# Kernel tuning notes

Hardware: AMD Instinct MI355X
Metric: run time of the kernel (lower is better)

## Reference

```python
import jax, jax.numpy as jnp
import numpy as np

E = 32          # n_routed_experts / num_local_experts
H = 1024        # hidden_size
I = 512         # moe_intermediate_size
G = 8           # n_group
TKG = 4         # topk_group
TOPK = 8        # num_experts_per_tok
NSH = 2         # n_shared_experts
SCALE = 2.5     # routed_scaling_factor


def setup_inputs() -> dict:
    key = jax.random.key(0)
    ks = jax.random.split(key, 10)
    s = 0.02
    return {
        "hidden_states": jax.random.normal(ks[0], (2, 1024, H), jnp.float32),
        # router: linear weight [E, H] and e_score_correction_bias [E]
        "gate_w": jax.random.normal(ks[1], (E, H), jnp.float32) * s,
        "gate_bias": jax.random.normal(ks[2], (E,), jnp.float32) * s,
        # routed experts (stacked SwiGLU weights, torch Linear layout [out, in])
        "w_gate": jax.random.normal(ks[3], (E, I, H), jnp.float32) * s,
        "w_up": jax.random.normal(ks[4], (E, I, H), jnp.float32) * s,
        "w_down": jax.random.normal(ks[5], (E, H, I), jnp.float32) * s,
        # shared experts: one MLP with intermediate = I * NSH
        "sh_gate": jax.random.normal(ks[6], (I * NSH, H), jnp.float32) * s,
        "sh_up": jax.random.normal(ks[7], (I * NSH, H), jnp.float32) * s,
        "sh_down": jax.random.normal(ks[8], (H, I * NSH), jnp.float32) * s,
    }


def reference(hidden_states, gate_w, gate_bias, w_gate, w_up, w_down,
              sh_gate, sh_up, sh_down):
    B, S, Hd = hidden_states.shape
    h = hidden_states.reshape(-1, Hd)                      # [T, H]

    # ---- router (DeepseekV3TopkRouter + route_tokens_to_experts) ----
    logits = h.astype(jnp.float32) @ gate_w.T              # [T, E]
    scores = jax.nn.sigmoid(logits)
    sc = scores + gate_bias                                # scores_for_choice
    # group score = sum of top-2 expert scores within each group
    grp = sc.reshape(-1, G, E // G)                        # [T, G, E/G]
    group_scores = jax.lax.top_k(grp, 2)[0].sum(-1)        # [T, G]
    gidx = jax.lax.top_k(group_scores, TKG)[1]             # [T, TKG]
    gmask = jnp.sum(jax.nn.one_hot(gidx, G, dtype=sc.dtype), axis=1)  # [T, G]
    smask = jnp.repeat(gmask, E // G, axis=1)              # [T, E]
    masked = jnp.where(smask > 0, sc, jnp.zeros_like(sc))  # masked_fill(~mask, 0)
    tki = jax.lax.top_k(masked, TOPK)[1]                   # [T, TOPK]
    tkw = jnp.take_along_axis(scores, tki, axis=1)         # gather raw sigmoid scores
    tkw = tkw / (tkw.sum(-1, keepdims=True) + 1e-20)       # norm_topk_prob
    tkw = tkw * SCALE

    # ---- dispatch-compute-combine (experts_forward) ----
    # combine[t, e] = sum_k tkw[t, k] * [tki[t, k] == e]
    combine = (jax.nn.one_hot(tki, E, dtype=tkw.dtype) * tkw[..., None]).sum(1)  # [T, E]
    g = jax.nn.silu(jnp.einsum('th,eih->tei', h, w_gate))  # [T, E, I]
    u = jnp.einsum('th,eih->tei', h, w_up)                 # [T, E, I]
    routed = jnp.einsum('tei,ehi->th', g * u * combine[:, :, None], w_down)  # [T, H]

    # ---- shared experts ----
    sg = jax.nn.silu(h @ sh_gate.T)
    shared = (sg * (h @ sh_up.T)) @ sh_down.T              # [T, H]

    return (routed + shared).reshape(B, S, Hd)
```

## Files before the change

### kernel.cpp

```cpp
#include <hip/hip_runtime.h>
#include <hip/hip_bf16.h>
#include <cstdint>

#define E_ 32
#define H_ 1024
#define I_ 512
#define G_ 8
#define NSH_ 2
#define SCALE_ 2.5f
#define NROUTED (E_ * I_)
#define PADCAP (16384 + E_ * 128)

typedef unsigned short u16;
using bf16x8_t = __attribute__((ext_vector_type(8))) __bf16;
using f32x4_t  = __attribute__((ext_vector_type(4))) float;

__device__ __forceinline__ u16 f2bf(float x) {
  union { float f; uint32_t u; } v; v.f = x;
  uint32_t u = v.u;
  uint32_t r = (u + 0x7fffu + ((u >> 16) & 1u)) >> 16;
  return (u16)r;
}
__device__ __forceinline__ float bf2f(u16 x) {
  union { uint32_t u; float f; } v; v.u = ((uint32_t)x) << 16; return v.f;
}

__device__ __forceinline__ void load_lds16(const void* g, void* l) {
  __builtin_amdgcn_global_load_lds(
      (const __attribute__((address_space(1))) unsigned int*)g,
      (__attribute__((address_space(3))) unsigned int*)l,
      16, 0, 0);
}

#define OFF_BU   16777216L
#define OFF_BD   33554432L
#define OFF_BSHG 50331648L
#define OFF_BSHU 51380224L
#define OFF_BSHD 52428800L
#define WBF_TOT  53477376L

#define W4_WG  4194304L
#define W4_WU  8388608L
#define W4_WD  12582912L
#define W4_SHG 12845056L
#define W4_SHU 13107200L
#define W4_TOT 13369344L
__global__ void prep_kernel(const float* __restrict__ gw, float* __restrict__ gwT,
                            int* __restrict__ counts, int* __restrict__ cursor,
                            int* __restrict__ qheads,
                            int* __restrict__ tok_list, float* __restrict__ wt_list,
                            const float* __restrict__ wg, const float* __restrict__ wu,
                            const float* __restrict__ wd, const float* __restrict__ shg,
                            const float* __restrict__ shu, const float* __restrict__ shd,
                            u16* __restrict__ wbf) {
  long i0 = (long)blockIdx.x * blockDim.x + threadIdx.x;
  if (i0 < H_ * E_) {
    int k = (int)(i0 >> 5), e = (int)(i0 & 31);
    gwT[i0] = gw[(long)e * H_ + k];
  }
  if (i0 < PADCAP) { tok_list[i0] = 0; wt_list[i0] = 0.f; }
  if (i0 < E_) { counts[i0] = 0; cursor[i0] = 0; }
  if (i0 < 2) qheads[i0] = 0;

  long stride = (long)gridDim.x * blockDim.x;
  for (long i = i0; i < W4_TOT; i += stride) {
    const float* s; long off; long dofs;
    if (i < W4_WG)       { s = wg;  off = i;            dofs = off * 4; }
    else if (i < W4_WU)  { s = wu;  off = i - W4_WG;    dofs = OFF_BU + off * 4; }
    else if (i < W4_WD)  { s = wd;  off = i - W4_WU;    dofs = OFF_BD + off * 4; }
    else if (i < W4_SHG) { s = shg; off = i - W4_WD;    dofs = OFF_BSHG + off * 4; }
    else if (i < W4_SHU) { s = shu; off = i - W4_SHG;   dofs = OFF_BSHU + off * 4; }
    else                 { s = shd; off = i - W4_SHU;   dofs = OFF_BSHD + off * 4; }
    float4 v = ((const float4*)s)[off];
    ushort4 o;
    o.x = f2bf(v.x); o.y = f2bf(v.y); o.z = f2bf(v.z); o.w = f2bf(v.w);
    *(ushort4*)(wbf + dofs) = o;
  }
}

__global__ __launch_bounds__(256) void logits_kernel(
    const float* __restrict__ h, const float* __restrict__ gwT,
    float* __restrict__ lpart,
    u16* __restrict__ hbf, int T) {
  __shared__ float shh[64][128];
  __shared__ float shw[128][E_];
  const int tid = threadIdx.x;
  const int t0 = blockIdx.x * 64;
  const int k0 = blockIdx.y * 128;
  #pragma unroll
  for (int i = 0; i < 8; ++i) {
    int c = tid + 256 * i;
    int row = c >> 5, col = c & 31;
    float4 v = *(const float4*)(h + (size_t)(t0 + row) * H_ + k0 + col * 4);
    *(float4*)(&shh[row][col * 4]) = v;
    ushort4 o;
    o.x = f2bf(v.x); o.y = f2bf(v.y); o.z = f2bf(v.z); o.w = f2bf(v.w);
    *(ushort4*)(hbf + (size_t)(t0 + row) * H_ + k0 + col * 4) = o;
  }
  #pragma unroll
  for (int i = 0; i < 4; ++i) {
    int c = tid + 256 * i;
    int row = c >> 3, col = c & 7;
    *(float4*)(&shw[row][col * 4]) =
        *(const float4*)(gwT + (size_t)(k0 + row) * E_ + col * 4);
  }
  __syncthreads();
  const int e = tid & 31;
  const int tb = (tid >> 5) * 8;
  float acc[8] = {0.f, 0.f, 0.f, 0.f, 0.f, 0.f, 0.f, 0.f};
  #pragma unroll 4
  for (int k = 0; k < 128; ++k) {
    float wv = shw[k][e];
    #pragma unroll
    for (int j = 0; j < 8; ++j) acc[j] += shh[tb + j][k] * wv;
  }
  #pragma unroll
  for (int j = 0; j < 8; ++j)
    lpart[((size_t)blockIdx.y * T + (t0 + tb + j)) * E_ + e] = acc[j];
}

__global__ __launch_bounds__(256) void topk_kernel(
    const float* __restrict__ lpart, const float* __restrict__ gb,
    int* __restrict__ idx8, float* __restrict__ wt8, int* __restrict__ counts,
    int T) {
  const int tid = threadIdx.x;
  const int l = tid & 63, wid = tid >> 6;
  const int e = l & 31, half = l >> 5;
  const int t = blockIdx.x * 8 + wid * 2 + half;

  float lg = 0.f;
  #pragma unroll
  for (int s = 0; s < 8; ++s) lg += lpart[((size_t)s * T + t) * E_ + e];
  float score = 1.f / (1.f + __expf(-lg));
  float sc = score + gb[e];

  float x1 = __shfl_xor(sc, 1);
  float x2 = __shfl_xor(sc, 2);
  float x3 = __shfl_xor(sc, 3);
  float hi1 = fmaxf(sc, x1), lo1 = fminf(sc, x1);
  float hi2 = fmaxf(x2, x3), lo2 = fminf(x2, x3);
  float m1 = fmaxf(hi1, hi2);
  float m2 = (hi1 >= hi2) ? fmaxf(lo1, hi2) : fmaxf(lo2, hi1);
  float gs = m1 + m2;

  float ga[8];
  #pragma unroll
  for (int g = 0; g < 8; ++g) ga[g] = __shfl(gs, (half << 5) + g * 4);
  unsigned gm = 0;
  #pragma unroll
  for (int r = 0; r < 4; ++r) {
    float bv = -1e30f; int bi = 0;
    #pragma unroll
    for (int g = 0; g < 8; ++g)
      if (!((gm >> g) & 1u) && ga[g] > bv) { bv = ga[g]; bi = g; }
    gm |= 1u << bi;
  }
  float msk = ((gm >> (e >> 2)) & 1u) ? sc : 0.f;

  float wsum = 0.f, myw = 0.f;
  int myi = 0;
  #pragma unroll
  for (int r = 0; r < 8; ++r) {
    float av = msk; int ai = e;
    #pragma unroll
    for (int m = 16; m; m >>= 1) {
      float ov = __shfl_xor(av, m);
      int oi = __shfl_xor(ai, m);
      if (ov > av || (ov == av && oi < ai)) { av = ov; ai = oi; }
    }
    float wscore = __shfl(score, (half << 5) + ai);
    wsum += wscore;
    if (e == r) { myi = ai; myw = wscore; }
    if (e == ai) msk = 0.f;
  }
  float inv = SCALE_ / (wsum + 1e-20f);
  if (e < 8) {
    idx8[(size_t)t * 8 + e] = myi;
    wt8[(size_t)t * 8 + e] = myw * inv;
    atomicAdd(&counts[myi], 1);
  }
}

__global__ void fill_kernel(const int* __restrict__ idx8, const float* __restrict__ wt8,
                            const int* __restrict__ counts, int* __restrict__ cursor,
                            int* __restrict__ tok_list, float* __restrict__ wt_list,
                            int* __restrict__ pair_pos, int npair) {
  int i = blockIdx.x * blockDim.x + threadIdx.x;
  if (i >= npair) return;
  int e = idx8[i];
  int offz = 0;
  for (int k = 0; k < E_; ++k) {
    if (k == e) break;
    offz += ((counts[k] + 127) >> 7) << 7;
  }
  int p = atomicAdd(&cursor[e], 1);
  int slot = offz + p;
  tok_list[slot] = i >> 3;
  wt_list[slot] = wt8[i];
  pair_pos[i] = slot;
}

__global__ __launch_bounds__(256, 2) void p1_kernel(
    const u16* __restrict__ hbf,
    const u16* __restrict__ wbf,
    const int* __restrict__ counts,
    const int* __restrict__ tok_list, const float* __restrict__ wt_list,
    int* __restrict__ qheads,
    u16* __restrict__ gu,
    u16* __restrict__ gu_sh,
    int T) {
  __shared__ u16 lsA[3][128 * 32];
  __shared__ u16 lsB0[3][128 * 32];
  __shared__ u16 lsB1[3][128 * 32];
  __shared__ int s_tok[128];
  __shared__ float s_wt[128];
  __shared__ int s_off[E_], s_ntt[E_];
  __shared__ int s_tot, s_tile;

  const int tid = threadIdx.x;
  if (tid == 0) {
    int run = 0, tot = 0;
    for (int e = 0; e < E_; ++e) {
      s_off[e] = run;
      int nt = (counts[e] + 127) >> 7;
      s_ntt[e] = nt;
      run += nt << 7;
      tot += nt * 4;
    }
    s_tot = tot + (T / 128) * 8;
  }

  const int w = tid >> 6, l = tid & 63;
  const int wr = w >> 1, wc = w & 1;
  const int lr = l & 15, lh = l >> 4;
  const int rdblk = (lh ^ ((lr >> 1) & 3)) << 3;

  const int c0 = tid, c1 = tid + 256;
  const int row0 = c0 >> 2, cb0 = c0 & 3, scb0 = cb0 ^ ((row0 >> 1) & 3);
  const int row1 = c1 >> 2, cb1 = c1 & 3, scb1 = cb1 ^ ((row1 >> 1) & 3);

  for (;;) {
    __syncthreads();
    if (tid == 0) s_tile = atomicAdd(&qheads[0], 1);
    __syncthreads();
    int q = s_tile;
    if (q >= s_tot) break;

    int z = 0, rem = q;
    for (; z < E_; ++z) { int t = s_ntt[z] * 4; if (rem < t) break; rem -= t; }
    const bool sh_e = (z == E_);
    int tt, nb;
    if (sh_e) { tt = rem >> 3; nb = rem & 7; }
    else      { tt = rem >> 2; nb = rem & 3; }
    const int off = sh_e ? 0 : s_off[z];

    if (tid < 128) {
      if (sh_e) { s_tok[tid] = tt * 128 + tid; s_wt[tid] = 1.0f; }
      else {
        int slot = off + tt * 128 + tid;
        s_tok[tid] = tok_list[slot];
        s_wt[tid] = wt_list[slot];
      }
    }
    __syncthreads();

    const u16* Bg = sh_e ? (wbf + OFF_BSHG + (size_t)(nb * 128) * H_)
                         : (wbf + ((size_t)z * I_ + nb * 128) * H_);
    const u16* Bu = sh_e ? (wbf + OFF_BSHU + (size_t)(nb * 128) * H_)
                         : (wbf + OFF_BU + ((size_t)z * I_ + nb * 128) * H_);
    const u16* A0 = hbf + (size_t)s_tok[row0] * H_ + scb0 * 8;
    const u16* A1 = hbf + (size_t)s_tok[row1] * H_ + scb1 * 8;

    f32x4_t acc0[4][4], acc1[4][4];
    #pragma unroll
    for (int m = 0; m < 4; ++m)
      #pragma unroll
      for (int n = 0; n < 4; ++n) {
        acc0[m][n] = (f32x4_t){0.f, 0.f, 0.f, 0.f};
        acc1[m][n] = (f32x4_t){0.f, 0.f, 0.f, 0.f};
      }

    auto stage = [&](int b, int ks) {
      int k0 = ks * 32;
      load_lds16(A0 + k0, (char*)&lsA[b][0] + c0 * 16);
      load_lds16(A1 + k0, (char*)&lsA[b][0] + c1 * 16);
      load_lds16(Bg + (size_t)row0 * H_ + k0 + scb0 * 8, (char*)&lsB0[b][0] + c0 * 16);
      load_lds16(Bg + (size_t)row1 * H_ + k0 + scb1 * 8, (char*)&lsB0[b][0] + c1 * 16);
      load_lds16(Bu + (size_t)row0 * H_ + k0 + scb0 * 8, (char*)&lsB1[b][0] + c0 * 16);
      load_lds16(Bu + (size_t)row1 * H_ + k0 + scb1 * 8, (char*)&lsB1[b][0] + c1 * 16);
    };
    auto compute = [&](int b) {
      bf16x8_t af[4], b0f[4], b1f[4];
      #pragma unroll
      for (int m = 0; m < 4; ++m)
        af[m] = *(const bf16x8_t*)(&lsA[b][0] + (wr * 64 + m * 16 + lr) * 32 + rdblk);
      #pragma unroll
      for (int n = 0; n < 4; ++n) {
        b0f[n] = *(const bf16x8_t*)(&lsB0[b][0] + (wc * 64 + n * 16 + lr) * 32 + rdblk);
        b1f[n] = *(const bf16x8_t*)(&lsB1[b][0] + (wc * 64 + n * 16 + lr) * 32 + rdblk);
      }
      #pragma unroll
      for (int m = 0; m < 4; ++m)
        #pragma unroll
        for (int n = 0; n < 4; ++n) {
          acc0[m][n] = __builtin_amdgcn_mfma_f32_16x16x32_bf16(af[m], b0f[n], acc0[m][n], 0, 0, 0);
          acc1[m][n] = __builtin_amdgcn_mfma_f32_16x16x32_bf16(af[m], b1f[n], acc1[m][n], 0, 0, 0);
        }
    };

    stage(0, 0);
    stage(1, 1);
    int b0 = 0, b1 = 1, b2 = 2;
    #pragma unroll 1
    for (int s = 0; s < 31; ++s) {
      asm volatile("s_waitcnt vmcnt(6)" ::: "memory");
      __builtin_amdgcn_s_barrier();
      compute(b0);
      if (s < 30) stage(b2, s + 2);
      int tb = b0; b0 = b1; b1 = b2; b2 = tb;
    }
    asm volatile("s_waitcnt vmcnt(0)" ::: "memory");
    __builtin_amdgcn_s_barrier();
    compute(b0);

    const int ldo = sh_e ? (I_ * NSH_) : I_;
    u16* outp = sh_e ? (gu_sh + (size_t)(tt * 128) * ldo + nb * 128)
                     : (gu + (size_t)(off + tt * 128) * ldo + nb * 128);
    #pragma unroll
    for (int m = 0; m < 4; ++m) {
      #pragma unroll
      for (int n = 0; n < 4; ++n) {
        int col = wc * 64 + n * 16 + lr;
        #pragma unroll
        for (int j = 0; j < 4; ++j) {
          int trow = wr * 64 + m * 16 + lh * 4 + j;
          float gv = acc0[m][n][j], uv = acc1[m][n][j];
          float sv = gv / (1.f + __expf(-gv));
          outp[(size_t)trow * ldo + col] = f2bf(sv * uv * s_wt[trow]);
        }
      }
    }
  }
}

__global__ __launch_bounds__(256, 3) void p2_kernel(
    const u16* __restrict__ gu, const u16* __restrict__ gu_sh,
    const u16* __restrict__ wbf,
    const int* __restrict__ counts,
    int* __restrict__ qheads,
    u16* __restrict__ part,
    u16* __restrict__ part_sh,
    int T) {
  __shared__ u16 lsA[3][128 * 32];
  __shared__ u16 lsB[3][128 * 32];
  __shared__ int s_off[E_], s_ntt[E_];
  __shared__ int s_tot, s_tile;

  const int tid = threadIdx.x;
  if (tid == 0) {
    int run = 0, tot = 0;
    for (int e = 0; e < E_; ++e) {
      s_off[e] = run;
      int nt = (counts[e] + 127) >> 7;
      s_ntt[e] = nt;
      run += nt << 7;
      tot += nt * 8;
    }
    s_tot = tot + (T / 128) * 8;
  }

  const int w = tid >> 6, l = tid & 63;
  const int wr = w >> 1, wc = w & 1;
  const int lr = l & 15, lh = l >> 4;
  const int rdblk = (lh ^ ((lr >> 1) & 3)) << 3;

  const int c0 = tid, c1 = tid + 256;
  const int row0 = c0 >> 2, cb0 = c0 & 3, scb0 = cb0 ^ ((row0 >> 1) & 3);
  const int row1 = c1 >> 2, cb1 = c1 & 3, scb1 = cb1 ^ ((row1 >> 1) & 3);

  for (;;) {
    __syncthreads();
    if (tid == 0) s_tile = atomicAdd(&qheads[1], 1);
    __syncthreads();
    int q = s_tile;
    if (q >= s_tot) break;

    int z = 0, rem = q;
    for (; z < E_; ++z) { int t = s_ntt[z] * 8; if (rem < t) break; rem -= t; }
    const bool sh_e = (z == E_);
    int tt = rem >> 3, nb = rem & 7;

    const int K = sh_e ? (I_ * NSH_) : I_;
    const int NT = K / 32;
    const u16* Ab = sh_e ? (gu_sh + (size_t)(tt * 128) * K)
                         : (gu + (size_t)(s_off[z] + tt * 128) * K);
    const u16* Bb = sh_e ? (wbf + OFF_BSHD + (size_t)(nb * 128) * K)
                         : (wbf + OFF_BD + (size_t)z * H_ * I_ + (size_t)(nb * 128) * K);
    u16* outp = sh_e ? (part_sh + (size_t)(tt * 128) * H_ + nb * 128)
                     : (part + (size_t)(s_off[z] + tt * 128) * H_ + nb * 128);

    f32x4_t acc[4][4];
    #pragma unroll
    for (int m = 0; m < 4; ++m)
      #pragma unroll
      for (int n = 0; n < 4; ++n) acc[m][n] = (f32x4_t){0.f, 0.f, 0.f, 0.f};

    auto stage = [&](int b, int ks) {
      int k0 = ks * 32;
      load_lds16(Ab + (size_t)row0 * K + k0 + scb0 * 8, (char*)&lsA[b][0] + c0 * 16);
      load_lds16(Ab + (size_t)row1 * K + k0 + scb1 * 8, (char*)&lsA[b][0] + c1 * 16);
      load_lds16(Bb + (size_t)row0 * K + k0 + scb0 * 8, (char*)&lsB[b][0] + c0 * 16);
      load_lds16(Bb + (size_t)row1 * K + k0 + scb1 * 8, (char*)&lsB[b][0] + c1 * 16);
    };
    auto compute = [&](int b) {
      bf16x8_t af[4], bf[4];
      #pragma unroll
      for (int m = 0; m < 4; ++m)
        af[m] = *(const bf16x8_t*)(&lsA[b][0] + (wr * 64 + m * 16 + lr) * 32 + rdblk);
      #pragma unroll
      for (int n = 0; n < 4; ++n)
        bf[n] = *(const bf16x8_t*)(&lsB[b][0] + (wc * 64 + n * 16 + lr) * 32 + rdblk);
      #pragma unroll
      for (int m = 0; m < 4; ++m)
        #pragma unroll
        for (int n = 0; n < 4; ++n)
          acc[m][n] = __builtin_amdgcn_mfma_f32_16x16x32_bf16(af[m], bf[n], acc[m][n], 0, 0, 0);
    };

    stage(0, 0);
    stage(1, 1);
    int b0 = 0, b1 = 1, b2 = 2;
    #pragma unroll 1
    for (int s = 0; s < NT - 1; ++s) {
      asm volatile("s_waitcnt vmcnt(4)" ::: "memory");
      __builtin_amdgcn_s_barrier();
      compute(b0);
      if (s + 2 < NT) stage(b2, s + 2);
      int tb = b0; b0 = b1; b1 = b2; b2 = tb;
    }
    asm volatile("s_waitcnt vmcnt(0)" ::: "memory");
    __builtin_amdgcn_s_barrier();
    compute(b0);

    #pragma unroll
    for (int m = 0; m < 4; ++m) {
      #pragma unroll
      for (int n = 0; n < 4; ++n) {
        int col = wc * 64 + n * 16 + lr;
        #pragma unroll
        for (int j = 0; j < 4; ++j) {
          int trow = wr * 64 + m * 16 + lh * 4 + j;
          outp[(size_t)trow * H_ + col] = f2bf(acc[m][n][j]);
        }
      }
    }
  }
}

__global__ void combine_kernel(const u16* __restrict__ part, const u16* __restrict__ part_sh,
                               const int* __restrict__ pair_pos, float* __restrict__ out) {
  int t = blockIdx.x;
  int h = threadIdx.x * 4;
  int pp[8];
  #pragma unroll
  for (int s = 0; s < 8; ++s) pp[s] = pair_pos[(long)t * 8 + s];
  ushort4 v = *(const ushort4*)(part_sh + (size_t)t * H_ + h);
  float a0 = bf2f(v.x), a1 = bf2f(v.y), a2 = bf2f(v.z), a3 = bf2f(v.w);
  #pragma unroll
  for (int s = 0; s < 8; ++s) {
    ushort4 u = *(const ushort4*)(part + (size_t)pp[s] * H_ + h);
    a0 += bf2f(u.x); a1 += bf2f(u.y); a2 += bf2f(u.z); a3 += bf2f(u.w);
  }
  float4 o = {a0, a1, a2, a3};
  *(float4*)(out + (size_t)t * H_ + h) = o;
}

extern "C" void kernel_launch(void* const* d_in, const int* in_sizes, int n_in,
                              void* d_out, int out_size, void* d_ws, size_t ws_size,
                              hipStream_t stream) {
  const float* hs  = (const float*)d_in[0];
  const float* gw  = (const float*)d_in[1];
  const float* gb  = (const float*)d_in[2];
  const float* wg  = (const float*)d_in[3];
  const float* wu  = (const float*)d_in[4];
  const float* wd  = (const float*)d_in[5];
  const float* shg = (const float*)d_in[6];
  const float* shu = (const float*)d_in[7];
  const float* shd = (const float*)d_in[8];
  float* out = (float*)d_out;

  const int T = in_sizes[0] / H_;

  char* ws = (char*)d_ws;
  size_t off = 0;
  auto alloc = [&](size_t bytes) {
    char* p = ws + off;
    off += (bytes + 255) & ~(size_t)255;
    return p;
  };
  int*   counts   = (int*)alloc(E_ * 4);
  int*   cursor   = (int*)alloc(E_ * 4);
  int*   qheads   = (int*)alloc(2 * 4);
  int*   idx8     = (int*)alloc((size_t)T * 8 * 4);
  float* wt8      = (float*)alloc((size_t)T * 8 * 4);
  int*   pair_pos = (int*)alloc((size_t)T * 8 * 4);
  int*   tok_list = (int*)alloc(PADCAP * 4);
  float* wt_list  = (float*)alloc(PADCAP * 4);
  float* gwT      = (float*)alloc((size_t)H_ * E_ * 4);
  float* lpart    = (float*)alloc((size_t)8 * T * E_ * 4);
  u16* hbf     = (u16*)alloc((size_t)T * H_ * 2);
  u16* wbf     = (u16*)alloc((size_t)WBF_TOT * 2);
  u16* gu      = (u16*)alloc((size_t)PADCAP * I_ * 2);
  u16* gu_sh   = (u16*)alloc((size_t)T * I_ * NSH_ * 2);
  u16* part    = (u16*)alloc((size_t)PADCAP * H_ * 2);
  u16* part_sh = (u16*)alloc((size_t)T * H_ * 2);
  if (off > ws_size) return;

  hipLaunchKernelGGL(prep_kernel, dim3(4096), dim3(256), 0, stream,
                     gw, gwT, counts, cursor, qheads, tok_list, wt_list,
                     wg, wu, wd, shg, shu, shd, wbf);

  hipLaunchKernelGGL(logits_kernel, dim3(T / 64, 8), dim3(256), 0, stream,
                     hs, gwT, lpart, hbf, T);

  hipLaunchKernelGGL(topk_kernel, dim3(T / 8), dim3(256), 0, stream,
                     lpart, gb, idx8, wt8, counts, T);

  hipLaunchKernelGGL(fill_kernel, dim3((T * 8 + 255) / 256), dim3(256), 0, stream,
                     idx8, wt8, counts, cursor, tok_list, wt_list, pair_pos, T * 8);

  hipLaunchKernelGGL(p1_kernel, dim3(512), dim3(256), 0, stream,
                     hbf, wbf, counts, tok_list, wt_list, qheads, gu, gu_sh, T);

  hipLaunchKernelGGL(p2_kernel, dim3(768), dim3(256), 0, stream,
                     gu, gu_sh, wbf, counts, qheads, part, part_sh, T);

  hipLaunchKernelGGL(combine_kernel, dim3(T), dim3(256), 0, stream,
                     part, part_sh, pair_pos, out);
}
```

Baseline: 266.4 us.

## Shrink p1 N-tile to 64 for occupancy; stage p2 epilogue through LDS

The gate/up GEMM kernel now uses 128x64 output tiles instead of 128x128. That halves accumulator registers and B-tile LDS, allows 3 blocks per CU, and launches more persistent blocks. Tile order is changed so tiles sharing the same weight slice are adjacent, which should improve L2 reuse. The down-projection epilogue writes accumulators into LDS and then does coalesced ushort4 stores, replacing scattered 2-byte stores; the price is extra barriers and more A-operand reloads per output.

```diff
diff --git a/kernel.cpp b/kernel.cpp
--- a/kernel.cpp
+++ b/kernel.cpp
@@ -200,7 +200,7 @@
   pair_pos[i] = slot;
 }
 
-__global__ __launch_bounds__(256, 2) void p1_kernel(
+__global__ __launch_bounds__(256, 3) void p1_kernel(
     const u16* __restrict__ hbf,
     const u16* __restrict__ wbf,
     const int* __restrict__ counts,
@@ -210,8 +210,8 @@
     u16* __restrict__ gu_sh,
     int T) {
   __shared__ u16 lsA[3][128 * 32];
-  __shared__ u16 lsB0[3][128 * 32];
-  __shared__ u16 lsB1[3][128 * 32];
+  __shared__ u16 lsB0[3][64 * 32];
+  __shared__ u16 lsB1[3][64 * 32];
   __shared__ int s_tok[128];
   __shared__ float s_wt[128];
   __shared__ int s_off[E_], s_ntt[E_];
@@ -225,9 +225,9 @@
       int nt = (counts[e] + 127) >> 7;
       s_ntt[e] = nt;
       run += nt << 7;
-      tot += nt * 4;
-    }
-    s_tot = tot + (T / 128) * 8;
+      tot += nt * 8;
+    }
+    s_tot = tot + (T / 128) * 16;
   }
 
   const int w = tid >> 6, l = tid & 63;
@@ -235,9 +235,8 @@
   const int lr = l & 15, lh = l >> 4;
   const int rdblk = (lh ^ ((lr >> 1) & 3)) << 3;
 
-  const int c0 = tid, c1 = tid + 256;
-  const int row0 = c0 >> 2, cb0 = c0 & 3, scb0 = cb0 ^ ((row0 >> 1) & 3);
-  const int row1 = c1 >> 2, cb1 = c1 & 3, scb1 = cb1 ^ ((row1 >> 1) & 3);
+  const int rA0 = tid >> 2,          cb0 = tid & 3, sc0 = cb0 ^ ((rA0 >> 1) & 3);
+  const int rA1 = (tid + 256) >> 2,  sc1 = cb0 ^ ((rA1 >> 1) & 3);
 
   for (;;) {
     __syncthreads();
@@ -247,11 +246,11 @@
     if (q >= s_tot) break;
 
     int z = 0, rem = q;
-    for (; z < E_; ++z) { int t = s_ntt[z] * 4; if (rem < t) break; rem -= t; }
+    for (; z < E_; ++z) { int t = s_ntt[z] * 8; if (rem < t) break; rem -= t; }
     const bool sh_e = (z == E_);
     int tt, nb;
-    if (sh_e) { tt = rem >> 3; nb = rem & 7; }
-    else      { tt = rem >> 2; nb = rem & 3; }
+    if (sh_e) { nb = rem >> 4; tt = rem & 15; }
+    else      { int nt = s_ntt[z]; nb = rem / nt; tt = rem - nb * nt; }
     const int off = sh_e ? 0 : s_off[z];
 
     if (tid < 128) {
@@ -264,45 +263,45 @@
     }
     __syncthreads();
 
-    const u16* Bg = sh_e ? (wbf + OFF_BSHG + (size_t)(nb * 128) * H_)
-                         : (wbf + ((size_t)z * I_ + nb * 128) * H_);
-    const u16* Bu = sh_e ? (wbf + OFF_BSHU + (size_t)(nb * 128) * H_)
-                         : (wbf + OFF_BU + ((size_t)z * I_ + nb * 128) * H_);
-    const u16* A0 = hbf + (size_t)s_tok[row0] * H_ + scb0 * 8;
-    const u16* A1 = hbf + (size_t)s_tok[row1] * H_ + scb1 * 8;
-
-    f32x4_t acc0[4][4], acc1[4][4];
+    const u16* Bg = sh_e ? (wbf + OFF_BSHG + (size_t)(nb * 64) * H_)
+                         : (wbf + ((size_t)z * I_ + nb * 64) * H_);
+    const u16* Bu = sh_e ? (wbf + OFF_BSHU + (size_t)(nb * 64) * H_)
+                         : (wbf + OFF_BU + ((size_t)z * I_ + nb * 64) * H_);
+    const u16* A0p = hbf + (size_t)s_tok[rA0] * H_ + sc0 * 8;
+    const u16* A1p = hbf + (size_t)s_tok[rA1] * H_ + sc1 * 8;
+    const u16* Bgp = Bg + (size_t)rA0 * H_ + sc0 * 8;
+    const u16* Bup = Bu + (size_t)rA0 * H_ + sc0 * 8;
+
+    f32x4_t acc0[4][2], acc1[4][2];
     #pragma unroll
     for (int m = 0; m < 4; ++m)
       #pragma unroll
-      for (int n = 0; n < 4; ++n) {
+      for (int n = 0; n < 2; ++n) {
         acc0[m][n] = (f32x4_t){0.f, 0.f, 0.f, 0.f};
         acc1[m][n] = (f32x4_t){0.f, 0.f, 0.f, 0.f};
       }
 
     auto stage = [&](int b, int ks) {
       int k0 = ks * 32;
-      load_lds16(A0 + k0, (char*)&lsA[b][0] + c0 * 16);
-      load_lds16(A1 + k0, (char*)&lsA[b][0] + c1 * 16);
-      load_lds16(Bg + (size_t)row0 * H_ + k0 + scb0 * 8, (char*)&lsB0[b][0] + c0 * 16);
-      load_lds16(Bg + (size_t)row1 * H_ + k0 + scb1 * 8, (char*)&lsB0[b][0] + c1 * 16);
-      load_lds16(Bu + (size_t)row0 * H_ + k0 + scb0 * 8, (char*)&lsB1[b][0] + c0 * 16);
-      load_lds16(Bu + (size_t)row1 * H_ + k0 + scb1 * 8, (char*)&lsB1[b][0] + c1 * 16);
+      load_lds16(A0p + k0, (char*)&lsA[b][0] + tid * 16);
+      load_lds16(A1p + k0, (char*)&lsA[b][0] + (tid + 256) * 16);
+      load_lds16(Bgp + k0, (char*)&lsB0[b][0] + tid * 16);
+      load_lds16(Bup + k0, (char*)&lsB1[b][0] + tid * 16);
     };
     auto compute = [&](int b) {
-      bf16x8_t af[4], b0f[4], b1f[4];
+      bf16x8_t af[4], b0f[2], b1f[2];
       #pragma unroll
       for (int m = 0; m < 4; ++m)
         af[m] = *(const bf16x8_t*)(&lsA[b][0] + (wr * 64 + m * 16 + lr) * 32 + rdblk);
       #pragma unroll
-      for (int n = 0; n < 4; ++n) {
-        b0f[n] = *(const bf16x8_t*)(&lsB0[b][0] + (wc * 64 + n * 16 + lr) * 32 + rdblk);
-        b1f[n] = *(const bf16x8_t*)(&lsB1[b][0] + (wc * 64 + n * 16 + lr) * 32 + rdblk);
+      for (int n = 0; n < 2; ++n) {
+        b0f[n] = *(const bf16x8_t*)(&lsB0[b][0] + (wc * 32 + n * 16 + lr) * 32 + rdblk);
+        b1f[n] = *(const bf16x8_t*)(&lsB1[b][0] + (wc * 32 + n * 16 + lr) * 32 + rdblk);
       }
       #pragma unroll
       for (int m = 0; m < 4; ++m)
         #pragma unroll
-        for (int n = 0; n < 4; ++n) {
+        for (int n = 0; n < 2; ++n) {
           acc0[m][n] = __builtin_amdgcn_mfma_f32_16x16x32_bf16(af[m], b0f[n], acc0[m][n], 0, 0, 0);
           acc1[m][n] = __builtin_amdgcn_mfma_f32_16x16x32_bf16(af[m], b1f[n], acc1[m][n], 0, 0, 0);
         }
@@ -313,7 +312,7 @@
     int b0 = 0, b1 = 1, b2 = 2;
     #pragma unroll 1
     for (int s = 0; s < 31; ++s) {
-      asm volatile("s_waitcnt vmcnt(6)" ::: "memory");
+      asm volatile("s_waitcnt vmcnt(4)" ::: "memory");
       __builtin_amdgcn_s_barrier();
       compute(b0);
       if (s < 30) stage(b2, s + 2);
@@ -324,13 +323,13 @@
     compute(b0);
 
     const int ldo = sh_e ? (I_ * NSH_) : I_;
-    u16* outp = sh_e ? (gu_sh + (size_t)(tt * 128) * ldo + nb * 128)
-                     : (gu + (size_t)(off + tt * 128) * ldo + nb * 128);
+    u16* outp = sh_e ? (gu_sh + (size_t)(tt * 128) * ldo + nb * 64)
+                     : (gu + (size_t)(off + tt * 128) * ldo + nb * 64);
     #pragma unroll
     for (int m = 0; m < 4; ++m) {
       #pragma unroll
-      for (int n = 0; n < 4; ++n) {
-        int col = wc * 64 + n * 16 + lr;
+      for (int n = 0; n < 2; ++n) {
+        int col = wc * 32 + n * 16 + lr;
         #pragma unroll
         for (int j = 0; j < 4; ++j) {
           int trow = wr * 64 + m * 16 + lh * 4 + j;
@@ -442,16 +441,29 @@
     __builtin_amdgcn_s_barrier();
     compute(b0);
 
-    #pragma unroll
-    for (int m = 0; m < 4; ++m) {
-      #pragma unroll
-      for (int n = 0; n < 4; ++n) {
-        int col = wc * 64 + n * 16 + lr;
+    u16* eb = &lsA[0][0];
+    #pragma unroll
+    for (int half = 0; half < 2; ++half) {
+      __syncthreads();
+      if (wr == half) {
         #pragma unroll
-        for (int j = 0; j < 4; ++j) {
-          int trow = wr * 64 + m * 16 + lh * 4 + j;
-          outp[(size_t)trow * H_ + col] = f2bf(acc[m][n][j]);
+        for (int m = 0; m < 4; ++m) {
+          #pragma unroll
+          for (int n = 0; n < 4; ++n) {
+            int col = wc * 64 + n * 16 + lr;
+            #pragma unroll
+            for (int j = 0; j < 4; ++j)
+              eb[(m * 16 + lh * 4 + j) * 128 + col] = f2bf(acc[m][n][j]);
+          }
         }
+      }
+      __syncthreads();
+      #pragma unroll
+      for (int i = 0; i < 8; ++i) {
+        int c = tid + 256 * i;
+        int row = c >> 5, col4 = c & 31;
+        *(ushort4*)(outp + (size_t)(half * 64 + row) * H_ + col4 * 4) =
+            *(const ushort4*)(eb + row * 128 + col4 * 4);
       }
     }
   }
@@ -529,7 +541,7 @@
   hipLaunchKernelGGL(fill_kernel, dim3((T * 8 + 255) / 256), dim3(256), 0, stream,
                      idx8, wt8, counts, cursor, tok_list, wt_list, pair_pos, T * 8);
 
-  hipLaunchKernelGGL(p1_kernel, dim3(512), dim3(256), 0, stream,
+  hipLaunchKernelGGL(p1_kernel, dim3(768), dim3(256), 0, stream,
                      hbf, wbf, counts, tok_list, wt_list, qheads, gu, gu_sh, T);
 
   hipLaunchKernelGGL(p2_kernel, dim3(768), dim3(256), 0, stream,
```

Result: slower. 283.3 us (+6.3%).
